# Kernel optimization log

Hardware: AMD Instinct MI355X
Metric: run time of the kernel (lower is better)

Reference implementation:

```python
import jax, jax.numpy as jnp
import numpy as np

NUM_CLASSES = 64
CDF_DIM = 128
EMBED_DIM = 1024
BATCH = 16


def setup_inputs() -> dict:
    key = jax.random.key(0)
    k_x, k_w1, k_b1, k_w2, k_b2 = jax.random.split(key, 5)
    bound1 = 1.0 / np.sqrt(EMBED_DIM)
    x = jax.random.normal(k_x, (BATCH, NUM_CLASSES * CDF_DIM, EMBED_DIM), dtype=jnp.float32)
    # stacked per-class weights: W1 [C,E,E] (applied as x @ W1), b1 [C,E], W2 [C,E], b2 [C]
    W1 = jax.random.uniform(k_w1, (NUM_CLASSES, EMBED_DIM, EMBED_DIM), jnp.float32, -bound1, bound1)
    b1 = jax.random.uniform(k_b1, (NUM_CLASSES, EMBED_DIM), jnp.float32, -bound1, bound1)
    W2 = jax.random.uniform(k_w2, (NUM_CLASSES, EMBED_DIM), jnp.float32, -bound1, bound1)
    b2 = jax.random.uniform(k_b2, (NUM_CLASSES,), jnp.float32, -bound1, bound1)
    return {"x": x, "W1": W1, "b1": b1, "W2": W2, "b2": b2}


def reference(x, W1, b1, W2, b2):
    B = x.shape[0]
    # [B, C, T, E] where T = cdf_dim
    xr = x.reshape(B, NUM_CLASSES, CDF_DIM, EMBED_DIM)
    # per-class first Linear + exact GELU (torch default is erf-based)
    h = jnp.einsum('bcte,ceo->bcto', xr, W1) + b1[None, :, None, :]
    h = jax.nn.gelu(h, approximate=False)
    # per-class second Linear to scalar, squeeze
    out = jnp.einsum('bcte,ce->bct', h, W2) + b2[None, :, None]
    # concat over classes -> [B, C*T]
    return out.reshape(B, NUM_CLASSES * CDF_DIM)
```

## Files before the change

kernel.cpp:

```cpp
#include <hip/hip_runtime.h>
#include <hip/hip_bf16.h>
#include <math.h>

#define NCLS 64
#define TDIM 128
#define EMB  1024
#define NBATCH 16

#define BM 128
#define BN 128
#define BK 32

typedef __attribute__((ext_vector_type(8))) short bfrag8;
typedef __attribute__((ext_vector_type(4))) float ffrag4;

__device__ __forceinline__ unsigned int pk2(float lo, float hi) {
    union { __hip_bfloat162 h; unsigned int u; } cv;
    cv.h = __float22bfloat162_rn(make_float2(lo, hi));
    return cv.u;
}
__device__ __forceinline__ short f2bs(float f) {
    return (short)(pk2(f, 0.f) & 0xffff);
}

union S8 { bfrag8 s; unsigned int u[4]; };

__device__ __forceinline__ void async16(const short* g, const short* l) {
    __builtin_amdgcn_global_load_lds(
        (const __attribute__((address_space(1))) unsigned int*)(unsigned long long)(uintptr_t)g,
        (__attribute__((address_space(3))) unsigned int*)(unsigned int)(uintptr_t)l,
        16, 0, 0);
}

__global__ __launch_bounds__(256) void init_out(const float* __restrict__ b2,
                                                float* __restrict__ out) {
    int i = blockIdx.x * 256 + threadIdx.x;
    int c = (i >> 7) & (NCLS - 1);
    out[i] = b2[c];
}

__global__ __launch_bounds__(256) void cvt_x(const float* __restrict__ x,
                                             short* __restrict__ xb) {
    size_t i = ((size_t)blockIdx.x * 256 + threadIdx.x) * 8;
    float4 a = *(const float4*)(x + i);
    float4 b = *(const float4*)(x + i + 4);
    S8 p;
    p.u[0] = pk2(a.x, a.y); p.u[1] = pk2(a.z, a.w);
    p.u[2] = pk2(b.x, b.y); p.u[3] = pk2(b.z, b.w);
    *(bfrag8*)(xb + i) = p.s;
}

__global__ __launch_bounds__(256) void cvt_w1t(const float* __restrict__ W1,
                                               short* __restrict__ w1t) {
    const int bid = blockIdx.x;
    const int nt = bid & 15, kt = (bid >> 4) & 15, c = bid >> 8;
    const int t = threadIdx.x;
    __shared__ short ldsT[64 * 72];

    const float* src = W1 + (size_t)c * 1048576 + (size_t)(kt * 64) * 1024 + nt * 64;
    const int kr = t >> 4, nq = (t & 15) * 4;
#pragma unroll
    for (int i = 0; i < 4; ++i) {
        int k = kr + i * 16;
        float4 v = *(const float4*)(src + (size_t)k * 1024 + nq);
        ldsT[(nq + 0) * 72 + k] = f2bs(v.x);
        ldsT[(nq + 1) * 72 + k] = f2bs(v.y);
        ldsT[(nq + 2) * 72 + k] = f2bs(v.z);
        ldsT[(nq + 3) * 72 + k] = f2bs(v.w);
    }
    __syncthreads();
    short* dst = w1t + (size_t)c * 1048576 + (size_t)(nt * 64) * 1024 + kt * 64;
#pragma unroll
    for (int p = 0; p < 2; ++p) {
        int chunk = t + p * 256;
        int n = chunk >> 3, kc = chunk & 7;
        bfrag8 v = *(const bfrag8*)(ldsT + n * 72 + kc * 8);
        *(bfrag8*)(dst + (size_t)n * 1024 + kc * 8) = v;
    }
}

__global__ __launch_bounds__(256) void mlp_gemm(
    const short* __restrict__ xb, const short* __restrict__ w1t,
    const float* __restrict__ b1, const float* __restrict__ W2,
    float* __restrict__ out)
{
    const int bid = blockIdx.x;
    const int xcd = bid & 7;
    const int idx = bid >> 3;
    const int c   = ((idx >> 7) << 3) | xcd;
    const int w   = idx & 127;
    const int mb  = w >> 3;
    const int nb  = w & 7;

    __shared__ __align__(16) short lds_a[2 * BM * BK];
    __shared__ __align__(16) short lds_b[2 * BN * BK];

    const int tid  = threadIdx.x;
    const int lane = tid & 63;
    const int wave = tid >> 6;
    const int wm = wave >> 1, wn = wave & 1;
    const int quad = lane >> 4, l16 = lane & 15;

    const short* gA0 = xb + ((size_t)mb * 8192 + c * 128 + (2 * wave) * 16 + l16) * 1024
                          + quad * 8;
    const short* gA1 = gA0 + 16 * 1024;
    const short* gB0 = w1t + (size_t)c * 1048576
                           + (size_t)(nb * 128 + (2 * wave) * 16 + l16) * 1024 + quad * 8;
    const short* gB1 = gB0 + 16 * 1024;
    const int stA = (2 * wave) * 512;

    ffrag4 acc[4][4] = {};

    async16(gA0, lds_a + stA);
    async16(gA1, lds_a + stA + 512);
    async16(gB0, lds_b + stA);
    async16(gB1, lds_b + stA + 512);
    gA0 += BK; gA1 += BK; gB0 += BK; gB1 += BK;
    __syncthreads();

    int cur = 0;
    for (int kt = 0; kt < EMB / BK; ++kt) {
        const short* la = lds_a + cur * (BM * BK);
        const short* lb = lds_b + cur * (BN * BK);

        if (kt + 1 < EMB / BK) {
            short* na = (short*)(lds_a + (cur ^ 1) * (BM * BK) + stA);
            short* nbp = (short*)(lds_b + (cur ^ 1) * (BN * BK) + stA);
            async16(gA0, na);
            async16(gA1, na + 512);
            async16(gB0, nbp);
            async16(gB1, nbp + 512);
            gA0 += BK; gA1 += BK; gB0 += BK; gB1 += BK;
        }

        const short* ard = la + (wm * 4) * 512 + quad * 128 + l16 * 8;
        const short* brd = lb + (wn * 4) * 512 + quad * 128 + l16 * 8;
        bfrag8 af[4], bf[4];
#pragma unroll
        for (int mi = 0; mi < 4; ++mi) af[mi] = *(const bfrag8*)(ard + mi * 512);
#pragma unroll
        for (int ni = 0; ni < 4; ++ni) bf[ni] = *(const bfrag8*)(brd + ni * 512);
#pragma unroll
        for (int mi = 0; mi < 4; ++mi)
#pragma unroll
            for (int ni = 0; ni < 4; ++ni)
                acc[mi][ni] = __builtin_amdgcn_mfma_f32_16x16x32_bf16(
                    af[mi], bf[ni], acc[mi][ni], 0, 0, 0);

        __syncthreads();
        cur ^= 1;
    }

    const int nbase = c * 1024 + nb * 128 + wn * 64 + l16;
    float b1v[4], w2v[4];
#pragma unroll
    for (int ni = 0; ni < 4; ++ni) {
        b1v[ni] = b1[nbase + ni * 16];
        w2v[ni] = W2[nbase + ni * 16];
    }

    float* outp = out + (size_t)mb * 8192 + c * 128 + wm * 64 + quad * 4;
#pragma unroll
    for (int mi = 0; mi < 4; ++mi) {
        float s[4] = {0.f, 0.f, 0.f, 0.f};
#pragma unroll
        for (int ni = 0; ni < 4; ++ni) {
#pragma unroll
            for (int r = 0; r < 4; ++r) {
                float h = acc[mi][ni][r] + b1v[ni];
                float g = 0.5f * h * (1.0f + erff(h * 0.70710678118654752f));
                s[r] += g * w2v[ni];
            }
        }
#pragma unroll
        for (int r = 0; r < 4; ++r) {
            s[r] += __shfl_xor(s[r], 8, 64);
            s[r] += __shfl_xor(s[r], 4, 64);
            s[r] += __shfl_xor(s[r], 2, 64);
            s[r] += __shfl_xor(s[r], 1, 64);
            if (l16 == 0) atomicAdd(outp + mi * 16 + r, s[r]);
        }
    }
}

__global__ __launch_bounds__(256) void mlp_head_fallback(
    const float* __restrict__ x,  const float* __restrict__ W1,
    const float* __restrict__ b1, const float* __restrict__ W2,
    float* __restrict__ out)
{
    const int bid = blockIdx.x;
    const int nb = bid & 7;
    const int mb = (bid >> 3) & 15;
    const int c  = bid >> 7;

    __shared__ __align__(16) short lds_a[BM * BK];
    __shared__ __align__(16) short lds_b[BN * BK];

    const int tid  = threadIdx.x;
    const int lane = tid & 63;
    const int wave = tid >> 6;
    const int wm = wave >> 1, wn = wave & 1;
    const int quad = lane >> 4, l16 = lane & 15;

    const int arow = tid & 127;
    const int akh  = tid >> 7;
    const float* aptr = x + ((size_t)mb * 8192 + (size_t)c * 128 + arow) * 1024 + akh * 16;
    short* aw0 = lds_a + (arow >> 4) * 512 + (akh * 2) * 128 + (arow & 15) * 8;
    short* aw1 = aw0 + 128;

    const int ncol = tid & 127;
    const int bkh  = tid >> 7;
    const float* bptr = W1 + (size_t)c * 1024 * 1024 + (size_t)(bkh * 16) * 1024
                           + (size_t)nb * 128 + ncol;
    short* bw0 = lds_b + (ncol >> 4) * 512 + (bkh * 2) * 128 + (ncol & 15) * 8;
    short* bw1 = bw0 + 128;

    const short* ard = lds_a + (wm * 4) * 512 + quad * 128 + l16 * 8;
    const short* brd = lds_b + (wn * 4) * 512 + quad * 128 + l16 * 8;

    ffrag4 acc[4][4] = {};

    for (int kt = 0; kt < EMB / BK; ++kt) {
        float4 a0 = *(const float4*)(aptr + 0);
        float4 a1 = *(const float4*)(aptr + 4);
        float4 a2 = *(const float4*)(aptr + 8);
        float4 a3 = *(const float4*)(aptr + 12);
        float bv[16];
#pragma unroll
        for (int j = 0; j < 16; ++j) bv[j] = bptr[(size_t)j * 1024];
        aptr += BK;
        bptr += (size_t)BK * 1024;

        __syncthreads();

        S8 pa0, pa1, pb0, pb1;
        pa0.u[0] = pk2(a0.x, a0.y); pa0.u[1] = pk2(a0.z, a0.w);
        pa0.u[2] = pk2(a1.x, a1.y); pa0.u[3] = pk2(a1.z, a1.w);
        pa1.u[0] = pk2(a2.x, a2.y); pa1.u[1] = pk2(a2.z, a2.w);
        pa1.u[2] = pk2(a3.x, a3.y); pa1.u[3] = pk2(a3.z, a3.w);
#pragma unroll
        for (int j = 0; j < 4; ++j) pb0.u[j] = pk2(bv[2 * j], bv[2 * j + 1]);
#pragma unroll
        for (int j = 0; j < 4; ++j) pb1.u[j] = pk2(bv[8 + 2 * j], bv[9 + 2 * j]);

        *(bfrag8*)aw0 = pa0.s;
        *(bfrag8*)aw1 = pa1.s;
        *(bfrag8*)bw0 = pb0.s;
        *(bfrag8*)bw1 = pb1.s;

        __syncthreads();

        bfrag8 af[4], bf[4];
#pragma unroll
        for (int mi = 0; mi < 4; ++mi) af[mi] = *(const bfrag8*)(ard + mi * 512);
#pragma unroll
        for (int ni = 0; ni < 4; ++ni) bf[ni] = *(const bfrag8*)(brd + ni * 512);
#pragma unroll
        for (int mi = 0; mi < 4; ++mi)
#pragma unroll
            for (int ni = 0; ni < 4; ++ni)
                acc[mi][ni] = __builtin_amdgcn_mfma_f32_16x16x32_bf16(
                    af[mi], bf[ni], acc[mi][ni], 0, 0, 0);
    }

    const int nbase = c * 1024 + nb * 128 + wn * 64 + l16;
    float b1v[4], w2v[4];
#pragma unroll
    for (int ni = 0; ni < 4; ++ni) {
        b1v[ni] = b1[nbase + ni * 16];
        w2v[ni] = W2[nbase + ni * 16];
    }

    float* outp = out + (size_t)mb * 8192 + c * 128 + wm * 64 + quad * 4;
#pragma unroll
    for (int mi = 0; mi < 4; ++mi) {
        float s[4] = {0.f, 0.f, 0.f, 0.f};
#pragma unroll
        for (int ni = 0; ni < 4; ++ni) {
#pragma unroll
            for (int r = 0; r < 4; ++r) {
                float h = acc[mi][ni][r] + b1v[ni];
                float g = 0.5f * h * (1.0f + erff(h * 0.70710678118654752f));
                s[r] += g * w2v[ni];
            }
        }
#pragma unroll
        for (int r = 0; r < 4; ++r) {
            s[r] += __shfl_xor(s[r], 8, 64);
            s[r] += __shfl_xor(s[r], 4, 64);
            s[r] += __shfl_xor(s[r], 2, 64);
            s[r] += __shfl_xor(s[r], 1, 64);
            if (l16 == 0) atomicAdd(outp + mi * 16 + r, s[r]);
        }
    }
}

extern "C" void kernel_launch(void* const* d_in, const int* in_sizes, int n_in,
                              void* d_out, int out_size, void* d_ws, size_t ws_size,
                              hipStream_t stream) {
    const float* x  = (const float*)d_in[0];
    const float* W1 = (const float*)d_in[1];
    const float* b1 = (const float*)d_in[2];
    const float* W2 = (const float*)d_in[3];
    const float* b2 = (const float*)d_in[4];
    float* out = (float*)d_out;

    const size_t xb_bytes  = (size_t)NBATCH * NCLS * TDIM * EMB * 2;
    const size_t w1t_bytes = (size_t)NCLS * EMB * EMB * 2;

    init_out<<<dim3(512), dim3(256), 0, stream>>>(b2, out);

    if (ws_size >= xb_bytes + w1t_bytes) {
        short* xb  = (short*)d_ws;
        short* w1t = (short*)((char*)d_ws + xb_bytes);
        cvt_x<<<dim3(65536), dim3(256), 0, stream>>>(x, xb);
        cvt_w1t<<<dim3(16384), dim3(256), 0, stream>>>(W1, w1t);
        mlp_gemm<<<dim3(NCLS * 16 * 8), dim3(256), 0, stream>>>(xb, w1t, b1, W2, out);
    } else {
        mlp_head_fallback<<<dim3(NCLS * 16 * 8), dim3(256), 0, stream>>>(x, W1, b1, W2, out);
    }
}
```

Measured before the change: 1.509 ms.

## Triple-buffer LDS pipeline with manual waitcnt and fast erf approximation for GELU

Replaces the double-buffered LDS k-loop with a three-stage ring buffer. Global loads run two tiles ahead, with explicit vmcnt/lgkmcnt waits, raw s_barrier and raised priority around the MFMA block, so memory latency is better hidden. It also adds an occupancy hint of 3 blocks per CU and swaps erff for an Abramowitz-Stegun polynomial erf approximation in the GELU epilogue. The approximation has about 1e-7 absolute error, which may slightly change accuracy against the exact-erf reference. The extra LDS buffer raises shared memory per block.

```diff
diff --git a/kernel.cpp b/kernel.cpp
--- a/kernel.cpp
+++ b/kernel.cpp
@@ -10,6 +10,8 @@
 #define BM 128
 #define BN 128
 #define BK 32
+#define NT (EMB / BK)
+#define BUFSH 8192
 
 typedef __attribute__((ext_vector_type(8))) short bfrag8;
 typedef __attribute__((ext_vector_type(4))) float ffrag4;
@@ -30,6 +32,19 @@
         (const __attribute__((address_space(1))) unsigned int*)(unsigned long long)(uintptr_t)g,
         (__attribute__((address_space(3))) unsigned int*)(unsigned int)(uintptr_t)l,
         16, 0, 0);
+}
+
+__device__ __forceinline__ float gelu_fast(float h) {
+    float az = fabsf(h) * 0.70710678118654752f;
+    float t  = __builtin_amdgcn_rcpf(fmaf(0.3275911f, az, 1.0f));
+    float p  = fmaf(1.061405429f, t, -1.453152027f);
+    p = fmaf(p, t, 1.421413741f);
+    p = fmaf(p, t, -0.284496736f);
+    p = fmaf(p, t, 0.254829592f);
+    p = p * t;
+    float e = __expf(-az * az);
+    float y = fmaf(-p, e, 1.0f);
+    return fmaf(0.5f * fabsf(h), y, 0.5f * h);
 }
 
 __global__ __launch_bounds__(256) void init_out(const float* __restrict__ b2,
@@ -79,7 +94,7 @@
     }
 }
 
-__global__ __launch_bounds__(256) void mlp_gemm(
+__global__ __launch_bounds__(256, 3) void mlp_gemm(
     const short* __restrict__ xb, const short* __restrict__ w1t,
     const float* __restrict__ b1, const float* __restrict__ W2,
     float* __restrict__ out)
@@ -92,8 +107,7 @@
     const int mb  = w >> 3;
     const int nb  = w & 7;
 
-    __shared__ __align__(16) short lds_a[2 * BM * BK];
-    __shared__ __align__(16) short lds_b[2 * BN * BK];
+    __shared__ __align__(16) short lds[3 * BUFSH];
 
     const int tid  = threadIdx.x;
     const int lane = tid & 63;
@@ -108,47 +122,62 @@
                            + (size_t)(nb * 128 + (2 * wave) * 16 + l16) * 1024 + quad * 8;
     const short* gB1 = gB0 + 16 * 1024;
     const int stA = (2 * wave) * 512;
+    const int stB = 4096 + (2 * wave) * 512;
+
+    const int ardo = (wm * 4) * 512 + quad * 128 + l16 * 8;
+    const int brdo = 4096 + (wn * 4) * 512 + quad * 128 + l16 * 8;
 
     ffrag4 acc[4][4] = {};
 
-    async16(gA0, lds_a + stA);
-    async16(gA1, lds_a + stA + 512);
-    async16(gB0, lds_b + stA);
-    async16(gB1, lds_b + stA + 512);
+    async16(gA0, lds + stA);        async16(gA1, lds + stA + 512);
+    async16(gB0, lds + stB);        async16(gB1, lds + stB + 512);
     gA0 += BK; gA1 += BK; gB0 += BK; gB1 += BK;
-    __syncthreads();
-
-    int cur = 0;
-    for (int kt = 0; kt < EMB / BK; ++kt) {
-        const short* la = lds_a + cur * (BM * BK);
-        const short* lb = lds_b + cur * (BN * BK);
-
-        if (kt + 1 < EMB / BK) {
-            short* na = (short*)(lds_a + (cur ^ 1) * (BM * BK) + stA);
-            short* nbp = (short*)(lds_b + (cur ^ 1) * (BN * BK) + stA);
-            async16(gA0, na);
-            async16(gA1, na + 512);
-            async16(gB0, nbp);
-            async16(gB1, nbp + 512);
+    async16(gA0, lds + BUFSH + stA); async16(gA1, lds + BUFSH + stA + 512);
+    async16(gB0, lds + BUFSH + stB); async16(gB1, lds + BUFSH + stB + 512);
+    gA0 += BK; gA1 += BK; gB0 += BK; gB1 += BK;
+    asm volatile("s_waitcnt vmcnt(4)" ::: "memory");
+    __builtin_amdgcn_sched_barrier(0);
+    __builtin_amdgcn_s_barrier();
+    __builtin_amdgcn_sched_barrier(0);
+
+    int qr = 0;
+    int qs = 2;
+    for (int t = 0; t < NT; ++t) {
+        if (t < NT - 2) {
+            const short* sb = lds + qs * BUFSH;
+            async16(gA0, sb + stA); async16(gA1, sb + stA + 512);
+            async16(gB0, sb + stB); async16(gB1, sb + stB + 512);
             gA0 += BK; gA1 += BK; gB0 += BK; gB1 += BK;
         }
-
-        const short* ard = la + (wm * 4) * 512 + quad * 128 + l16 * 8;
-        const short* brd = lb + (wn * 4) * 512 + quad * 128 + l16 * 8;
+        const short* rb = lds + qr * BUFSH;
         bfrag8 af[4], bf[4];
 #pragma unroll
-        for (int mi = 0; mi < 4; ++mi) af[mi] = *(const bfrag8*)(ard + mi * 512);
-#pragma unroll
-        for (int ni = 0; ni < 4; ++ni) bf[ni] = *(const bfrag8*)(brd + ni * 512);
+        for (int mi = 0; mi < 4; ++mi) af[mi] = *(const bfrag8*)(rb + ardo + mi * 512);
+#pragma unroll
+        for (int ni = 0; ni < 4; ++ni) bf[ni] = *(const bfrag8*)(rb + brdo + ni * 512);
+        asm volatile("s_waitcnt lgkmcnt(0)" ::: "memory");
+        __builtin_amdgcn_sched_barrier(0);
+        __builtin_amdgcn_s_setprio(1);
 #pragma unroll
         for (int mi = 0; mi < 4; ++mi)
 #pragma unroll
             for (int ni = 0; ni < 4; ++ni)
                 acc[mi][ni] = __builtin_amdgcn_mfma_f32_16x16x32_bf16(
                     af[mi], bf[ni], acc[mi][ni], 0, 0, 0);
-
-        __syncthreads();
-        cur ^= 1;
+        __builtin_amdgcn_s_setprio(0);
+        __builtin_amdgcn_sched_barrier(0);
+        if (t < NT - 2) {
+            asm volatile("s_waitcnt vmcnt(4)" ::: "memory");
+        } else if (t == NT - 2) {
+            asm volatile("s_waitcnt vmcnt(0)" ::: "memory");
+        }
+        if (t < NT - 1) {
+            __builtin_amdgcn_sched_barrier(0);
+            __builtin_amdgcn_s_barrier();
+            __builtin_amdgcn_sched_barrier(0);
+        }
+        qr = (qr == 2) ? 0 : qr + 1;
+        qs = (qs == 2) ? 0 : qs + 1;
     }
 
     const int nbase = c * 1024 + nb * 128 + wn * 64 + l16;
@@ -168,8 +197,7 @@
 #pragma unroll
             for (int r = 0; r < 4; ++r) {
                 float h = acc[mi][ni][r] + b1v[ni];
-                float g = 0.5f * h * (1.0f + erff(h * 0.70710678118654752f));
-                s[r] += g * w2v[ni];
+                s[r] += gelu_fast(h) * w2v[ni];
             }
         }
 #pragma unroll
@@ -280,8 +308,7 @@
 #pragma unroll
             for (int r = 0; r < 4; ++r) {
                 float h = acc[mi][ni][r] + b1v[ni];
-                float g = 0.5f * h * (1.0f + erff(h * 0.70710678118654752f));
-                s[r] += g * w2v[ni];
+                s[r] += gelu_fast(h) * w2v[ni];
             }
         }
 #pragma unroll
```

New measurement: 1.396 ms. -7.5%, faster.
